# Kernel optimization log

Measured on AMD Instinct MI355X. Metric: run time of the kernel, lower is better.

Reference implementation:

```python
import jax, jax.numpy as jnp
import numpy as np

E, P, T, B = 512, 128, 1024, 1


def _lstm_dir(x, wih, whh, bih, bhh, reverse):
    # x: [B, T, Din]; torch LSTM gate order: i, f, g, o
    Bb = x.shape[0]
    H = whh.shape[1]
    xg = jnp.einsum('btd,gd->btg', x, wih) + bih + bhh  # [B, T, 4H]
    xg = jnp.swapaxes(xg, 0, 1)  # [T, B, 4H]

    def step(carry, g_t):
        h, c = carry
        g = g_t + h @ whh.T
        i, f, gg, o = jnp.split(g, 4, axis=-1)
        c = jax.nn.sigmoid(f) * c + jax.nn.sigmoid(i) * jnp.tanh(gg)
        h = jax.nn.sigmoid(o) * jnp.tanh(c)
        return (h, c), h

    h0 = jnp.zeros((Bb, H), x.dtype)
    _, hs = jax.lax.scan(step, (h0, h0), xg, reverse=reverse)
    return jnp.swapaxes(hs, 0, 1)  # [B, T, H]


def _bilstm(x, layers):
    for wih, whh, bih, bhh in layers:
        f = _lstm_dir(x, wih[0], whh[0], bih[0], bhh[0], False)
        b = _lstm_dir(x, wih[1], whh[1], bih[1], bhh[1], True)
        x = jnp.concatenate([f, b], axis=-1)
    return x


def setup_inputs() -> dict:
    key = jax.random.key(0)
    ks = jax.random.split(key, 20)
    s = 0.05
    d = {
        'words': jax.random.normal(ks[0], (B, T, E), jnp.float32),
        'pos': jax.random.normal(ks[1], (B, T, P), jnp.float32),
        'w_w0_ih': s * jax.random.normal(ks[2], (2, 4 * E, E), jnp.float32),
        'w_w0_hh': s * jax.random.normal(ks[3], (2, 4 * E, E), jnp.float32),
        'w_b0_ih': s * jax.random.normal(ks[4], (2, 4 * E), jnp.float32),
        'w_b0_hh': s * jax.random.normal(ks[5], (2, 4 * E), jnp.float32),
        'w_w1_ih': s * jax.random.normal(ks[6], (2, 4 * E, 2 * E), jnp.float32),
        'w_w1_hh': s * jax.random.normal(ks[7], (2, 4 * E, E), jnp.float32),
        'w_b1_ih': s * jax.random.normal(ks[8], (2, 4 * E), jnp.float32),
        'w_b1_hh': s * jax.random.normal(ks[9], (2, 4 * E), jnp.float32),
        'p_w0_ih': s * jax.random.normal(ks[10], (2, 4 * P, P), jnp.float32),
        'p_w0_hh': s * jax.random.normal(ks[11], (2, 4 * P, P), jnp.float32),
        'p_b0_ih': s * jax.random.normal(ks[12], (2, 4 * P), jnp.float32),
        'p_b0_hh': s * jax.random.normal(ks[13], (2, 4 * P), jnp.float32),
        'p_w1_ih': s * jax.random.normal(ks[14], (2, 4 * P, 2 * P), jnp.float32),
        'p_w1_hh': s * jax.random.normal(ks[15], (2, 4 * P, P), jnp.float32),
        'p_b1_ih': s * jax.random.normal(ks[16], (2, 4 * P), jnp.float32),
        'p_b1_hh': s * jax.random.normal(ks[17], (2, 4 * P), jnp.float32),
        'edge_w': s * jax.random.normal(ks[18], (1, 4 * (E + P)), jnp.float32),
        'edge_b': s * jax.random.normal(ks[19], (1,), jnp.float32),
    }
    return d


def reference(words, pos, w_w0_ih, w_w0_hh, w_b0_ih, w_b0_hh, w_w1_ih, w_w1_hh,
              w_b1_ih, w_b1_hh, p_w0_ih, p_w0_hh, p_b0_ih, p_b0_hh, p_w1_ih,
              p_w1_hh, p_b1_ih, p_b1_hh, edge_w, edge_b):
    hw = _bilstm(words, [(w_w0_ih, w_w0_hh, w_b0_ih, w_b0_hh),
                         (w_w1_ih, w_w1_hh, w_b1_ih, w_b1_hh)])  # [B,T,2E]
    hp = _bilstm(pos, [(p_w0_ih, p_w0_hh, p_b0_ih, p_b0_hh),
                       (p_w1_ih, p_w1_hh, p_b1_ih, p_b1_hh)])    # [B,T,2P]
    H = jnp.concatenate([hw, hp], axis=-1)[0]  # [T, 2(E+P)]
    D = H.shape[-1]
    # edge_scorer(concat(h_i, h_j)) = h_i @ W1 + h_j @ W2 + b
    s1 = H @ edge_w[0, :D]  # [T]
    s2 = H @ edge_w[0, D:]  # [T]
    S = s1[:, None] + s2[None, :] + edge_b[0]
    n = H.shape[0]
    eye = jnp.eye(n, dtype=bool)
    return jnp.where(eye, jnp.zeros((), S.dtype), S)  # diagonal stays 0
```

## Files before the change

### kernel.cpp

```cpp
#include <hip/hip_runtime.h>


#define T_LEN 1024

__global__ void poison_kernel(unsigned* p, int n) {
  int i = blockIdx.x * blockDim.x + threadIdx.x;
  int stride = gridDim.x * blockDim.x;
  for (; i < n; i += stride) p[i] = 0xFFFFFFFFu;
}

__global__ __launch_bounds__(256) void gemm_bt(
    const float* __restrict__ A,
    const float* __restrict__ Wt,
    const float* __restrict__ B0,
    const float* __restrict__ B1,
    float* __restrict__ C,
    int M, int N, int K)
{
  const int z = blockIdx.z;
  const float* W  = Wt + (size_t)z * N * K;
  const float* b0 = B0 + (size_t)z * N;
  const float* b1 = B1 + (size_t)z * N;
  float* Cz = C + (size_t)z * M * N;

  __shared__ __align__(16) float As[16][64];
  __shared__ __align__(16) float Ws[16][64];

  const int tid = threadIdx.x;
  const int tx = tid & 15, ty = tid >> 4;
  const int brow = blockIdx.y * 64, bcol = blockIdx.x * 64;
  const int lr = tid >> 2;
  const int lk = (tid & 3) << 2;

  float acc[4][4] = {};

  for (int k0 = 0; k0 < K; k0 += 16) {
    float4 av = *(const float4*)(A + (size_t)(brow + lr) * K + k0 + lk);
    float4 wv = *(const float4*)(W + (size_t)(bcol + lr) * K + k0 + lk);
    __syncthreads();
    As[lk + 0][lr] = av.x; As[lk + 1][lr] = av.y;
    As[lk + 2][lr] = av.z; As[lk + 3][lr] = av.w;
    Ws[lk + 0][lr] = wv.x; Ws[lk + 1][lr] = wv.y;
    Ws[lk + 2][lr] = wv.z; Ws[lk + 3][lr] = wv.w;
    __syncthreads();
    #pragma unroll
    for (int kk = 0; kk < 16; ++kk) {
      float4 a = *(const float4*)&As[kk][ty << 2];
      float4 w = *(const float4*)&Ws[kk][tx << 2];
      float a4[4] = {a.x, a.y, a.z, a.w};
      float w4[4] = {w.x, w.y, w.z, w.w};
      #pragma unroll
      for (int i = 0; i < 4; ++i)
        #pragma unroll
        for (int j = 0; j < 4; ++j)
          acc[i][j] = fmaf(a4[i], w4[j], acc[i][j]);
    }
  }

  const int nb = bcol + (tx << 2);
  float bias[4];
  #pragma unroll
  for (int j = 0; j < 4; ++j) bias[j] = b0[nb + j] + b1[nb + j];
  #pragma unroll
  for (int i = 0; i < 4; ++i) {
    int m = brow + (ty << 2) + i;
    float4 out;
    out.x = acc[i][0] + bias[0];
    out.y = acc[i][1] + bias[1];
    out.z = acc[i][2] + bias[2];
    out.w = acc[i][3] + bias[3];
    *(float4*)(Cz + (size_t)m * N + nb) = out;
  }
}

__device__ __forceinline__ float fsigmoid(float x) {
  return 1.f / (1.f + __expf(-x));
}
__device__ __forceinline__ float ftanh(float x) {
  return 2.f / (1.f + __expf(-2.f * x)) - 1.f;
}

template<int CTRL>
__device__ __forceinline__ float dpp_add(float v) {
  int x = __builtin_amdgcn_update_dpp(0, __float_as_int(v), CTRL, 0xf, 0xf, true);
  return v + __int_as_float(x);
}

__device__ __forceinline__ void word_body(
    int wg, const float* __restrict__ xg, const float* __restrict__ whh,
    float* hbuf, int rev)
{
  const int tid  = threadIdx.x;
  const int wave = tid >> 6;
  const int lane = tid & 63;
  const int p    = lane & 31;
  const int half = lane >> 5;
  const int eloc = wave * 2 + half;
  const int e    = wg * 16 + eloc;

  float4 wv[4][4];
  #pragma unroll
  for (int g = 0; g < 4; ++g) {
    const float* row = whh + (size_t)(g * 512 + e) * 512 + 4 * p;
    #pragma unroll
    for (int k = 0; k < 4; ++k)
      wv[g][k] = *(const float4*)(row + 128 * k);
  }

  __shared__ __align__(16) float h_lds[512];
  __shared__ __align__(16) float4 hgates[16];

  unsigned* hb = (unsigned*)hbuf;

  const bool tail = (tid < 16);
  float cst = 0.f;
  float xg4[4] = {0.f, 0.f, 0.f, 0.f};
  if (tail) {
    const int t0 = rev ? (T_LEN - 1) : 0;
    #pragma unroll
    for (int g = 0; g < 4; ++g)
      xg4[g] = xg[(size_t)t0 * 2048 + g * 512 + wg * 16 + tid];
  }

  unsigned A = 0, B = 0, C = 0;

  for (int s = 0; s < T_LEN; ++s) {
    const int t = rev ? (T_LEN - 1 - s) : s;

    if (s == 0) {
      h_lds[tid] = 0.f;
    } else {
      const int tp = rev ? (t + 1) : (t - 1);
      const unsigned* addr = hb + (size_t)tp * 512 + tid;
      asm volatile(
          "s_waitcnt vmcnt(0)\n\t"
          "global_load_dword %0, %3, off sc0 sc1\n\t"
          "global_load_dword %1, %3, off sc0 sc1\n\t"
          "global_load_dword %2, %3, off sc0 sc1\n\t"
          "Lpoll%=:\n\t"
          "s_waitcnt vmcnt(2)\n\t"
          "v_cmp_eq_u32 vcc, -1, %0\n\t"
          "s_cbranch_vccz Ldone%=\n\t"
          "global_load_dword %0, %3, off sc0 sc1\n\t"
          "s_waitcnt vmcnt(2)\n\t"
          "v_cmp_eq_u32 vcc, -1, %1\n\t"
          "s_cbranch_vccz LuseB%=\n\t"
          "global_load_dword %1, %3, off sc0 sc1\n\t"
          "s_waitcnt vmcnt(2)\n\t"
          "v_cmp_eq_u32 vcc, -1, %2\n\t"
          "s_cbranch_vccz LuseC%=\n\t"
          "global_load_dword %2, %3, off sc0 sc1\n\t"
          "s_branch Lpoll%=\n\t"
          "LuseB%=:\n\t"
          "v_mov_b32 %0, %1\n\t"
          "s_branch Ldone%=\n\t"
          "LuseC%=:\n\t"
          "v_mov_b32 %0, %2\n\t"
          "Ldone%=:"
          : "+v"(A), "+v"(B), "+v"(C)
          : "v"(addr)
          : "vcc", "memory");
      h_lds[tid] = __uint_as_float(A);
    }
    __syncthreads();

    float a0 = 0.f, a1 = 0.f, a2 = 0.f, a3 = 0.f;
    #pragma unroll
    for (int k = 0; k < 4; ++k) {
      float4 hv = *(const float4*)&h_lds[128 * k + 4 * p];
      float h4[4] = {hv.x, hv.y, hv.z, hv.w};
      #pragma unroll
      for (int j = 0; j < 4; ++j) {
        a0 = fmaf(((const float*)&wv[0][k])[j], h4[j], a0);
        a1 = fmaf(((const float*)&wv[1][k])[j], h4[j], a1);
        a2 = fmaf(((const float*)&wv[2][k])[j], h4[j], a2);
        a3 = fmaf(((const float*)&wv[3][k])[j], h4[j], a3);
      }
    }

    a0 = dpp_add<0xB1>(a0);  a1 = dpp_add<0xB1>(a1);
    a2 = dpp_add<0xB1>(a2);  a3 = dpp_add<0xB1>(a3);
    a0 = dpp_add<0x4E>(a0);  a1 = dpp_add<0x4E>(a1);
    a2 = dpp_add<0x4E>(a2);  a3 = dpp_add<0x4E>(a3);
    a0 = dpp_add<0x141>(a0); a1 = dpp_add<0x141>(a1);
    a2 = dpp_add<0x141>(a2); a3 = dpp_add<0x141>(a3);
    a0 = dpp_add<0x140>(a0); a1 = dpp_add<0x140>(a1);
    a2 = dpp_add<0x140>(a2); a3 = dpp_add<0x140>(a3);
    a0 = dpp_add<0x142>(a0); a1 = dpp_add<0x142>(a1);
    a2 = dpp_add<0x142>(a2); a3 = dpp_add<0x142>(a3);

    if (p == 16) {
      float4 gsum; gsum.x = a0; gsum.y = a1; gsum.z = a2; gsum.w = a3;
      hgates[eloc] = gsum;
    }
    __syncthreads();

    if (tail) {
      float4 g4 = hgates[tid];
      float si = fsigmoid(g4.x + xg4[0]);
      float sf = fsigmoid(g4.y + xg4[1]);
      float tg = ftanh  (g4.z + xg4[2]);
      float so = fsigmoid(g4.w + xg4[3]);
      cst = fmaf(sf, cst, si * tg);
      float h = so * ftanh(cst);
      __hip_atomic_store(hb + (size_t)t * 512 + wg * 16 + tid,
                         __float_as_uint(h),
                         __ATOMIC_RELAXED, __HIP_MEMORY_SCOPE_AGENT);
      if (s + 1 < T_LEN) {
        const int tn = rev ? (t - 1) : (t + 1);
        #pragma unroll
        for (int g = 0; g < 4; ++g)
          xg4[g] = xg[(size_t)tn * 2048 + g * 512 + wg * 16 + tid];
      }
    }
  }

  asm volatile("s_waitcnt vmcnt(0)" : "+v"(A), "+v"(B), "+v"(C) :: "memory");
}

__device__ __forceinline__ void pos_body(
    const float* __restrict__ xg, const float* __restrict__ whh,
    float* __restrict__ hbuf, int rev)
{
  const int tid = threadIdx.x;
  const int p   = tid & 3;
  const int e   = tid >> 2;

  float w[4][32];
  #pragma unroll
  for (int g = 0; g < 4; ++g) {
    const float* row = whh + (size_t)(g * 128 + e) * 128 + 4 * p;
    #pragma unroll
    for (int k = 0; k < 8; ++k) {
      float4 v = *(const float4*)(row + 16 * k);
      w[g][k * 4 + 0] = v.x; w[g][k * 4 + 1] = v.y;
      w[g][k * 4 + 2] = v.z; w[g][k * 4 + 3] = v.w;
    }
  }

  __shared__ __align__(16) float h_lds[2][128];
  unsigned* hb = (unsigned*)hbuf;

  float cst = 0.f;
  float xg4[4] = {0.f, 0.f, 0.f, 0.f};
  if (p == 0) {
    const int t0 = rev ? (T_LEN - 1) : 0;
    #pragma unroll
    for (int g = 0; g < 4; ++g) xg4[g] = xg[(size_t)t0 * 512 + g * 128 + e];
  }
  if (tid < 128) h_lds[0][tid] = 0.f;
  __syncthreads();

  for (int s = 0; s < T_LEN; ++s) {
    const int t   = rev ? (T_LEN - 1 - s) : s;
    const int buf = s & 1;

    float a0 = 0.f, a1 = 0.f, a2 = 0.f, a3 = 0.f;
    #pragma unroll
    for (int k = 0; k < 8; ++k) {
      float4 hv = *(const float4*)&h_lds[buf][16 * k + 4 * p];
      float h4[4] = {hv.x, hv.y, hv.z, hv.w};
      #pragma unroll
      for (int j = 0; j < 4; ++j) {
        a0 = fmaf(w[0][k * 4 + j], h4[j], a0);
        a1 = fmaf(w[1][k * 4 + j], h4[j], a1);
        a2 = fmaf(w[2][k * 4 + j], h4[j], a2);
        a3 = fmaf(w[3][k * 4 + j], h4[j], a3);
      }
    }
    a0 = dpp_add<0xB1>(a0); a1 = dpp_add<0xB1>(a1);
    a2 = dpp_add<0xB1>(a2); a3 = dpp_add<0xB1>(a3);
    a0 = dpp_add<0x4E>(a0); a1 = dpp_add<0x4E>(a1);
    a2 = dpp_add<0x4E>(a2); a3 = dpp_add<0x4E>(a3);

    if (p == 0) {
      float si = fsigmoid(a0 + xg4[0]);
      float sf = fsigmoid(a1 + xg4[1]);
      float tg = ftanh  (a2 + xg4[2]);
      float so = fsigmoid(a3 + xg4[3]);
      cst = fmaf(sf, cst, si * tg);
      float h = so * ftanh(cst);
      h_lds[buf ^ 1][e] = h;
      __hip_atomic_store(hb + (size_t)t * 128 + e, __float_as_uint(h),
                         __ATOMIC_RELAXED, __HIP_MEMORY_SCOPE_AGENT);
      if (s + 1 < T_LEN) {
        const int tn = rev ? (t - 1) : (t + 1);
        #pragma unroll
        for (int g = 0; g < 4; ++g)
          xg4[g] = xg[(size_t)tn * 512 + g * 128 + e];
      }
    }
    __syncthreads();
  }
}

__device__ const int rtorder[16] = {7,8,6,9,5,10,4,11,3,12,2,13,1,14,0,15};

__device__ __forceinline__ void wait_rows(const unsigned* rowF,
                                          const unsigned* rowB, int width) {
  const int tid = threadIdx.x;
  if (tid < width) {
    while (__hip_atomic_load(rowF + tid, __ATOMIC_RELAXED,
                             __HIP_MEMORY_SCOPE_AGENT) == 0xFFFFFFFFu)
      __builtin_amdgcn_s_sleep(8);
    while (__hip_atomic_load(rowB + tid, __ATOMIC_RELAXED,
                             __HIP_MEMORY_SCOPE_AGENT) == 0xFFFFFFFFu)
      __builtin_amdgcn_s_sleep(8);
  }
  __syncthreads();
}

__device__ __forceinline__ void df_tile(
    const float* __restrict__ Alo, const float* __restrict__ Ahi, int ksplit,
    int K, const float* __restrict__ W,
    const float* __restrict__ b0, const float* __restrict__ b1,
    float* __restrict__ C, int N, int brow, int bcol)
{
  __shared__ __align__(16) float As[16][64];
  __shared__ __align__(16) float Ws[16][64];

  const int tid = threadIdx.x;
  const int tx = tid & 15, ty = (tid >> 4) & 15;
  const int lr = (tid >> 2) & 63;
  const int lk = (tid & 3) << 2;

  float acc[4][4] = {};

  for (int k0 = 0; k0 < K; k0 += 16) {
    float4 av, wv;
    if (tid < 256) {
      const int k = k0 + lk;
      const float* arow = (k < ksplit)
          ? (Alo + (size_t)(brow + lr) * ksplit + k)
          : (Ahi + (size_t)(brow + lr) * ksplit + (k - ksplit));
      av = *(const float4*)arow;
      wv = *(const float4*)(W + (size_t)(bcol + lr) * K + k0 + lk);
    }
    __syncthreads();
    if (tid < 256) {
      As[lk + 0][lr] = av.x; As[lk + 1][lr] = av.y;
      As[lk + 2][lr] = av.z; As[lk + 3][lr] = av.w;
      Ws[lk + 0][lr] = wv.x; Ws[lk + 1][lr] = wv.y;
      Ws[lk + 2][lr] = wv.z; Ws[lk + 3][lr] = wv.w;
    }
    __syncthreads();
    if (tid < 256) {
      #pragma unroll
      for (int kk = 0; kk < 16; ++kk) {
        float4 a = *(const float4*)&As[kk][ty << 2];
        float4 w = *(const float4*)&Ws[kk][tx << 2];
        float a4[4] = {a.x, a.y, a.z, a.w};
        float w4[4] = {w.x, w.y, w.z, w.w};
        #pragma unroll
        for (int i = 0; i < 4; ++i)
          #pragma unroll
          for (int j = 0; j < 4; ++j)
            acc[i][j] = fmaf(a4[i], w4[j], acc[i][j]);
      }
    }
  }

  if (tid < 256) {
    const int nb = bcol + (tx << 2);
    float bias[4];
    #pragma unroll
    for (int j = 0; j < 4; ++j) bias[j] = b0[nb + j] + b1[nb + j];
    #pragma unroll
    for (int i = 0; i < 4; ++i) {
      int m = brow + (ty << 2) + i;
      float4 out;
      out.x = acc[i][0] + bias[0];
      out.y = acc[i][1] + bias[1];
      out.z = acc[i][2] + bias[2];
      out.w = acc[i][3] + bias[3];
      *(float4*)(C + (size_t)m * N + nb) = out;
    }
  }
}

__global__ __launch_bounds__(512, 1) void rec_kernel(
    const float* xg_wf, const float* xg_wb, const float* whh_w,
    float* h_wf, float* h_wb,
    const float* xg_pf, const float* xg_pb, const float* whh_p,
    float* h_pf, float* h_pb,
    const float* w1_ih, const float* w1_b0, const float* w1_b1, float* xg1_w,
    const float* p1_ih, const float* p1_b0, const float* p1_b1, float* xg1_p)
{
  const int b = blockIdx.x;
  if (b < 32) {
    word_body(b, xg_wf, whh_w, h_wf, 0);
  } else if (b < 64) {
    word_body(b - 32, xg_wb, whh_w + 2048 * 512, h_wb, 1);
  } else if (b == 64) {
    pos_body(xg_pf, whh_p, h_pf, 0);
  } else if (b == 65) {
    pos_body(xg_pb, whh_p + 512 * 128, h_pb, 1);
  } else if (b < 194) {
    const int g = b - 66;
    for (int j = g; j < 1024; j += 128) {
      const int rti = rtorder[j >> 6];
      const int rem = j & 63;
      const int z = rem >> 5, ct = rem & 31;
      const int brow = rti * 64, bcol = ct * 64;
      wait_rows((const unsigned*)(h_wf + (size_t)(brow + 63) * 512),
                (const unsigned*)(h_wb + (size_t)brow * 512), 512);
      df_tile(h_wf, h_wb, 512, 1024,
              w1_ih + (size_t)z * 2048 * 1024,
              w1_b0 + z * 2048, w1_b1 + z * 2048,
              xg1_w + (size_t)z * 1024 * 2048, 2048, brow, bcol);
    }
  } else {
    const int g = b - 194;
    for (int j = g; j < 256; j += 8) {
      const int rti = rtorder[j >> 4];
      const int rem = j & 15;
      const int z = rem >> 3, ct = rem & 7;
      const int brow = rti * 64, bcol = ct * 64;
      wait_rows((const unsigned*)(h_pf + (size_t)(brow + 63) * 128),
                (const unsigned*)(h_pb + (size_t)brow * 128), 128);
      df_tile(h_pf, h_pb, 128, 256,
              p1_ih + (size_t)z * 512 * 256,
              p1_b0 + z * 512, p1_b1 + z * 512,
              xg1_p + (size_t)z * 1024 * 512, 512, brow, bcol);
    }
  }
}

__global__ __launch_bounds__(256) void edge_s(
    const float* __restrict__ hwf, const float* __restrict__ hwb,
    const float* __restrict__ hpf, const float* __restrict__ hpb,
    const float* __restrict__ ew, float* s1, float* s2)
{
  const int i = blockIdx.x;
  const int tid = threadIdx.x;
  float a1 = 0.f, a2 = 0.f;
  for (int d = tid; d < 1280; d += 256) {
    float hv;
    if (d < 512)       hv = hwf[i * 512 + d];
    else if (d < 1024) hv = hwb[i * 512 + d - 512];
    else if (d < 1152) hv = hpf[i * 128 + d - 1024];
    else               hv = hpb[i * 128 + d - 1152];
    a1 = fmaf(hv, ew[d], a1);
    a2 = fmaf(hv, ew[1280 + d], a2);
  }
  #pragma unroll
  for (int off = 32; off > 0; off >>= 1) {
    a1 += __shfl_xor(a1, off, 64);
    a2 += __shfl_xor(a2, off, 64);
  }
  __shared__ float r1[4], r2[4];
  const int wid = tid >> 6;
  if ((tid & 63) == 0) { r1[wid] = a1; r2[wid] = a2; }
  __syncthreads();
  if (tid == 0) {
    s1[i] = (r1[0] + r1[1]) + (r1[2] + r1[3]);
    s2[i] = (r2[0] + r2[1]) + (r2[2] + r2[3]);
  }
}

__global__ __launch_bounds__(256) void sfill(
    const float* __restrict__ s1, const float* __restrict__ s2,
    const float* __restrict__ eb, float* __restrict__ out)
{
  int e = blockIdx.x * 256 + threadIdx.x;
  int i = e >> 10, j = e & 1023;
  out[e] = (i == j) ? 0.f : s1[i] + s2[j] + eb[0];
}

extern "C" void kernel_launch(void* const* d_in, const int* in_sizes, int n_in,
                              void* d_out, int out_size, void* d_ws, size_t ws_size,
                              hipStream_t stream)
{
  const float* words   = (const float*)d_in[0];
  const float* pos     = (const float*)d_in[1];
  const float* w_w0_ih = (const float*)d_in[2];
  const float* w_w0_hh = (const float*)d_in[3];
  const float* w_b0_ih = (const float*)d_in[4];
  const float* w_b0_hh = (const float*)d_in[5];
  const float* w_w1_ih = (const float*)d_in[6];
  const float* w_w1_hh = (const float*)d_in[7];
  const float* w_b1_ih = (const float*)d_in[8];
  const float* w_b1_hh = (const float*)d_in[9];
  const float* p_w0_ih = (const float*)d_in[10];
  const float* p_w0_hh = (const float*)d_in[11];
  const float* p_b0_ih = (const float*)d_in[12];
  const float* p_b0_hh = (const float*)d_in[13];
  const float* p_w1_ih = (const float*)d_in[14];
  const float* p_w1_hh = (const float*)d_in[15];
  const float* p_b1_ih = (const float*)d_in[16];
  const float* p_b1_hh = (const float*)d_in[17];
  const float* edge_w  = (const float*)d_in[18];
  const float* edge_b  = (const float*)d_in[19];

  float* ws = (float*)d_ws;
  float* xg_w  = ws;
  float* xg_p  = ws + 4194304;
  float* hw0_f = ws + 5242880;
  float* hw0_b = hw0_f + 524288;
  float* hw1_f = hw0_b + 524288;
  float* hw1_b = hw1_f + 524288;
  float* hp0_f = hw1_b + 524288;
  float* hp0_b = hp0_f + 131072;
  float* hp1_f = hp0_b + 131072;
  float* hp1_b = hp1_f + 131072;
  float* s1    = hp1_b + 131072;
  float* s2    = s1 + 1024;

  poison_kernel<<<1024, 256, 0, stream>>>((unsigned*)hw0_f, 2359296);

  gemm_bt<<<dim3(32, 16, 2), 256, 0, stream>>>(words, w_w0_ih, w_b0_ih, w_b0_hh,
                                               xg_w, 1024, 2048, 512);
  gemm_bt<<<dim3(8, 16, 2), 256, 0, stream>>>(pos, p_w0_ih, p_b0_ih, p_b0_hh,
                                              xg_p, 1024, 512, 128);

  rec_kernel<<<202, 512, 0, stream>>>(
      xg_w, xg_w + 2097152, w_w0_hh, hw0_f, hw0_b,
      xg_p, xg_p + 524288, p_w0_hh, hp0_f, hp0_b,
      w_w1_ih, w_b1_ih, w_b1_hh, xg_w,
      p_w1_ih, p_b1_ih, p_b1_hh, xg_p);

  rec_kernel<<<66, 512, 0, stream>>>(
      xg_w, xg_w + 2097152, w_w1_hh, hw1_f, hw1_b,
      xg_p, xg_p + 524288, p_w1_hh, hp1_f, hp1_b,
      w_w1_ih, w_b1_ih, w_b1_hh, xg_w,
      p_w1_ih, p_b1_ih, p_b1_hh, xg_p);

  edge_s<<<1024, 256, 0, stream>>>(hw1_f, hw1_b, hp1_f, hp1_b, edge_w, s1, s2);
  sfill<<<4096, 256, 0, stream>>>(s1, s2, edge_b, (float*)d_out);
}
```

Baseline: 3.249 ms.

## Fuse edge score dot products into second recurrent kernel and pad shared tiles

Moves the per-row edge scorer dot products into extra blocks of the layer-1 recurrent kernel; these blocks spin on the hidden-state rows and compute s1/s2 as soon as each 64-row chunk is finished. This overlaps the edge work with the recurrence and removes a separate kernel launch, at the cost of extra spinning blocks and a larger poison fill. It also pads the shared-memory tiles of the GEMM routines to 68 columns to reduce bank conflicts.

```diff
diff --git a/kernel.cpp b/kernel.cpp
--- a/kernel.cpp
+++ b/kernel.cpp
@@ -23,8 +23,8 @@
   const float* b1 = B1 + (size_t)z * N;
   float* Cz = C + (size_t)z * M * N;
 
-  __shared__ __align__(16) float As[16][64];
-  __shared__ __align__(16) float Ws[16][64];
+  __shared__ __align__(16) float As[16][68];
+  __shared__ __align__(16) float Ws[16][68];
 
   const int tid = threadIdx.x;
   const int tx = tid & 15, ty = tid >> 4;
@@ -316,8 +316,8 @@
     const float* __restrict__ b0, const float* __restrict__ b1,
     float* __restrict__ C, int N, int brow, int bcol)
 {
-  __shared__ __align__(16) float As[16][64];
-  __shared__ __align__(16) float Ws[16][64];
+  __shared__ __align__(16) float As[16][68];
+  __shared__ __align__(16) float Ws[16][68];
 
   const int tid = threadIdx.x;
   const int tx = tid & 15, ty = (tid >> 4) & 15;
@@ -378,13 +378,47 @@
   }
 }
 
+__device__ __forceinline__ void edge_block(
+    int r, const float* __restrict__ hwf, const float* __restrict__ hwb,
+    const float* __restrict__ hpf, const float* __restrict__ hpb,
+    const float* __restrict__ ew, float* s1, float* s2)
+{
+  wait_rows((const unsigned*)(hwf + (size_t)(r * 64 + 63) * 512),
+            (const unsigned*)(hwb + (size_t)(r * 64) * 512), 512);
+  wait_rows((const unsigned*)(hpf + (size_t)(r * 64 + 63) * 128),
+            (const unsigned*)(hpb + (size_t)(r * 64) * 128), 128);
+  const int tid  = threadIdx.x;
+  const int wv   = tid >> 6;
+  const int lane = tid & 63;
+  for (int rr = wv; rr < 64; rr += 8) {
+    const int i = r * 64 + rr;
+    float a1 = 0.f, a2 = 0.f;
+    for (int d = lane; d < 1280; d += 64) {
+      float hv;
+      if (d < 512)       hv = hwf[i * 512 + d];
+      else if (d < 1024) hv = hwb[i * 512 + d - 512];
+      else if (d < 1152) hv = hpf[i * 128 + d - 1024];
+      else               hv = hpb[i * 128 + d - 1152];
+      a1 = fmaf(hv, ew[d], a1);
+      a2 = fmaf(hv, ew[1280 + d], a2);
+    }
+    #pragma unroll
+    for (int off = 32; off > 0; off >>= 1) {
+      a1 += __shfl_xor(a1, off, 64);
+      a2 += __shfl_xor(a2, off, 64);
+    }
+    if (lane == 0) { s1[i] = a1; s2[i] = a2; }
+  }
+}
+
 __global__ __launch_bounds__(512, 1) void rec_kernel(
     const float* xg_wf, const float* xg_wb, const float* whh_w,
     float* h_wf, float* h_wb,
     const float* xg_pf, const float* xg_pb, const float* whh_p,
     float* h_pf, float* h_pb,
     const float* w1_ih, const float* w1_b0, const float* w1_b1, float* xg1_w,
-    const float* p1_ih, const float* p1_b0, const float* p1_b1, float* xg1_p)
+    const float* p1_ih, const float* p1_b0, const float* p1_b1, float* xg1_p,
+    const float* ew, float* s1, float* s2, int mode)
 {
   const int b = blockIdx.x;
   if (b < 32) {
@@ -395,66 +429,38 @@
     pos_body(xg_pf, whh_p, h_pf, 0);
   } else if (b == 65) {
     pos_body(xg_pb, whh_p + 512 * 128, h_pb, 1);
-  } else if (b < 194) {
-    const int g = b - 66;
-    for (int j = g; j < 1024; j += 128) {
-      const int rti = rtorder[j >> 6];
-      const int rem = j & 63;
-      const int z = rem >> 5, ct = rem & 31;
-      const int brow = rti * 64, bcol = ct * 64;
-      wait_rows((const unsigned*)(h_wf + (size_t)(brow + 63) * 512),
-                (const unsigned*)(h_wb + (size_t)brow * 512), 512);
-      df_tile(h_wf, h_wb, 512, 1024,
-              w1_ih + (size_t)z * 2048 * 1024,
-              w1_b0 + z * 2048, w1_b1 + z * 2048,
-              xg1_w + (size_t)z * 1024 * 2048, 2048, brow, bcol);
+  } else if (mode == 0) {
+    if (b < 194) {
+      const int g = b - 66;
+      for (int j = g; j < 1024; j += 128) {
+        const int rti = rtorder[j >> 6];
+        const int rem = j & 63;
+        const int z = rem >> 5, ct = rem & 31;
+        const int brow = rti * 64, bcol = ct * 64;
+        wait_rows((const unsigned*)(h_wf + (size_t)(brow + 63) * 512),
+                  (const unsigned*)(h_wb + (size_t)brow * 512), 512);
+        df_tile(h_wf, h_wb, 512, 1024,
+                w1_ih + (size_t)z * 2048 * 1024,
+                w1_b0 + z * 2048, w1_b1 + z * 2048,
+                xg1_w + (size_t)z * 1024 * 2048, 2048, brow, bcol);
+      }
+    } else {
+      const int g = b - 194;
+      for (int j = g; j < 256; j += 8) {
+        const int rti = rtorder[j >> 4];
+        const int rem = j & 15;
+        const int z = rem >> 3, ct = rem & 7;
+        const int brow = rti * 64, bcol = ct * 64;
+        wait_rows((const unsigned*)(h_pf + (size_t)(brow + 63) * 128),
+                  (const unsigned*)(h_pb + (size_t)brow * 128), 128);
+        df_tile(h_pf, h_pb, 128, 256,
+                p1_ih + (size_t)z * 512 * 256,
+                p1_b0 + z * 512, p1_b1 + z * 512,
+                xg1_p + (size_t)z * 1024 * 512, 512, brow, bcol);
+      }
     }
   } else {
-    const int g = b - 194;
-    for (int j = g; j < 256; j += 8) {
-      const int rti = rtorder[j >> 4];
-      const int rem = j & 15;
-      const int z = rem >> 3, ct = rem & 7;
-      const int brow = rti * 64, bcol = ct * 64;
-      wait_rows((const unsigned*)(h_pf + (size_t)(brow + 63) * 128),
-                (const unsigned*)(h_pb + (size_t)brow * 128), 128);
-      df_tile(h_pf, h_pb, 128, 256,
-              p1_ih + (size_t)z * 512 * 256,
-              p1_b0 + z * 512, p1_b1 + z * 512,
-              xg1_p + (size_t)z * 1024 * 512, 512, brow, bcol);
-    }
-  }
-}
-
-__global__ __launch_bounds__(256) void edge_s(
-    const float* __restrict__ hwf, const float* __restrict__ hwb,
-    const float* __restrict__ hpf, const float* __restrict__ hpb,
-    const float* __restrict__ ew, float* s1, float* s2)
-{
-  const int i = blockIdx.x;
-  const int tid = threadIdx.x;
-  float a1 = 0.f, a2 = 0.f;
-  for (int d = tid; d < 1280; d += 256) {
-    float hv;
-    if (d < 512)       hv = hwf[i * 512 + d];
-    else if (d < 1024) hv = hwb[i * 512 + d - 512];
-    else if (d < 1152) hv = hpf[i * 128 + d - 1024];
-    else               hv = hpb[i * 128 + d - 1152];
-    a1 = fmaf(hv, ew[d], a1);
-    a2 = fmaf(hv, ew[1280 + d], a2);
-  }
-  #pragma unroll
-  for (int off = 32; off > 0; off >>= 1) {
-    a1 += __shfl_xor(a1, off, 64);
-    a2 += __shfl_xor(a2, off, 64);
-  }
-  __shared__ float r1[4], r2[4];
-  const int wid = tid >> 6;
-  if ((tid & 63) == 0) { r1[wid] = a1; r2[wid] = a2; }
-  __syncthreads();
-  if (tid == 0) {
-    s1[i] = (r1[0] + r1[1]) + (r1[2] + r1[3]);
-    s2[i] = (r2[0] + r2[1]) + (r2[2] + r2[3]);
+    edge_block(b - 66, h_wf, h_wb, h_pf, h_pb, ew, s1, s2);
   }
 }
 
@@ -506,7 +512,7 @@
   float* s1    = hp1_b + 131072;
   float* s2    = s1 + 1024;
 
-  poison_kernel<<<1024, 256, 0, stream>>>((unsigned*)hw0_f, 2359296);
+  poison_kernel<<<1024, 256, 0, stream>>>((unsigned*)hw0_f, 2621440);
 
   gemm_bt<<<dim3(32, 16, 2), 256, 0, stream>>>(words, w_w0_ih, w_b0_ih, w_b0_hh,
                                                xg_w, 1024, 2048, 512);
@@ -517,14 +523,15 @@
       xg_w, xg_w + 2097152, w_w0_hh, hw0_f, hw0_b,
       xg_p, xg_p + 524288, p_w0_hh, hp0_f, hp0_b,
       w_w1_ih, w_b1_ih, w_b1_hh, xg_w,
-      p_w1_ih, p_b1_ih, p_b1_hh, xg_p);
-
-  rec_kernel<<<66, 512, 0, stream>>>(
+      p_w1_ih, p_b1_ih, p_b1_hh, xg_p,
+      edge_w, s1, s2, 0);
+
+  rec_kernel<<<82, 512, 0, stream>>>(
       xg_w, xg_w + 2097152, w_w1_hh, hw1_f, hw1_b,
       xg_p, xg_p + 524288, p_w1_hh, hp1_f, hp1_b,
       w_w1_ih, w_b1_ih, w_b1_hh, xg_w,
-      p_w1_ih, p_b1_ih, p_b1_hh, xg_p);
-
-  edge_s<<<1024, 256, 0, stream>>>(hw1_f, hw1_b, hp1_f, hp1_b, edge_w, s1, s2);
+      p_w1_ih, p_b1_ih, p_b1_hh, xg_p,
+      edge_w, s1, s2, 1);
+
   sfill<<<4096, 256, 0, stream>>>(s1, s2, edge_b, (float*)d_out);
 }
```

Measured after the change: 3.293 ms. Within noise of the previous version (+1.4%).
